# Performance work log

Hardware: AMD Instinct MI355X
Metric: run time of the kernel (lower is better)

The kernel has to match this reference:

```python
import jax, jax.numpy as jnp
import numpy as np

HX_INIT = 1e-6  # matches torch: zeros + 1e-06


def log_g(x):
    # log of continuous activation g: x>=0 -> log(x+0.5), else log(sigmoid(x)) = -softplus(-x)
    return jnp.where(x >= 0, jnp.log(jax.nn.relu(x) + 0.5), -jax.nn.softplus(-x))


def setup_inputs() -> dict:
    key = jax.random.key(0)
    k1, k2, k3 = jax.random.split(key, 3)
    N, L, H_in, H = 8, 4096, 512, 512
    x = jax.random.normal(k1, (N, L, H_in), dtype=jnp.float32)
    W = jax.random.normal(k2, (3 * H, H_in), dtype=jnp.float32) * 0.05
    b = jax.random.normal(k3, (3 * H,), dtype=jnp.float32) * 0.05
    return {"x": x, "W": W, "b": b}


def reference(x, W, b):
    N, L, _ = x.shape
    H = W.shape[0] // 3
    # gate preactivations: (N, L, 3H)
    pre = jnp.einsum('nli,oi->nlo', x, W) + b
    f_pre, i_pre, h_pre = jnp.split(pre, 3, axis=-1)
    # log-space gates
    diff = jax.nn.softplus(-f_pre) - jax.nn.softplus(-i_pre)
    log_f = -jax.nn.softplus(diff)       # log f'_t
    log_i = -jax.nn.softplus(-diff)      # log i'_t
    log_tilde_h = log_g(h_pre)
    # initial hidden state hx = 1e-6 (zeros + eps), shape (N, 1, H)
    log_h0 = jnp.full((N, 1, H), jnp.log(jnp.asarray(HX_INIT, x.dtype)), dtype=x.dtype)
    log_values = jnp.concatenate([log_h0, log_i + log_tilde_h], axis=1)  # (N, L+1, H)
    # Heinsen log-space parallel scan
    a_star = jnp.pad(jnp.cumsum(log_f, axis=1), ((0, 0), (1, 0), (0, 0)))  # (N, L+1, H)
    log_h = a_star + jax.lax.cumlogsumexp(log_values - a_star, axis=1)
    return jnp.exp(log_h)[:, 1:]  # (N, L, H)
```

## Files before the change

### kernel.cpp

```cpp
#include <hip/hip_runtime.h>
#include <hip/hip_bf16.h>


#define H_DIM 512
#define LSEQ 4096
#define NBATCH 8
#define M_TOTAL (NBATCH * LSEQ)

#define BM 128
#define BK 64

#define CS 128
#define NC 32

typedef __attribute__((ext_vector_type(8))) short short8;
typedef __attribute__((ext_vector_type(4))) float floatx4;
typedef __attribute__((ext_vector_type(4))) float float4v;
typedef _Float16 h2 __attribute__((ext_vector_type(2)));
typedef _Float16 h4 __attribute__((ext_vector_type(4)));
typedef __attribute__((ext_vector_type(2))) float float2v;

#define NEG_BIG (-1.0e30f)
#define C_LOG2E 1.4426950408889634f
#define LOG2_HX0 (-19.931568569324174f)

__device__ __forceinline__ float exp2_hw(float x) {
#if __has_builtin(__builtin_amdgcn_exp2f)
    return __builtin_amdgcn_exp2f(x);
#else
    return exp2f(x);
#endif
}

__device__ __forceinline__ float log2_hw(float x) {
#if __has_builtin(__builtin_amdgcn_logf)
    return __builtin_amdgcn_logf(x);
#else
    return log2f(x);
#endif
}

__device__ __forceinline__ float logaddexp2_f(float p, float q) {
    float m = fmaxf(p, q);
    float d = -fabsf(p - q);
    return m + log2_hw(1.0f + exp2_hw(d));
}

__device__ __forceinline__ float bf16u_to_f(unsigned short u) {
    unsigned int w = ((unsigned int)u) << 16;
    float f;
    __builtin_memcpy(&f, &w, 4);
    return f;
}

__device__ __forceinline__ unsigned short f_to_bf16u(float f) {
    __hip_bfloat16 h = __float2bfloat16(f);
    unsigned short u;
    __builtin_memcpy(&u, &h, 2);
    return u;
}

__device__ __forceinline__ void gload_lds16(const void* g, void* l) {
    __builtin_amdgcn_global_load_lds(
        (const __attribute__((address_space(1))) unsigned int*)g,
        (__attribute__((address_space(3))) unsigned int*)l, 16, 0, 0);
}

__global__ void detect_and_bias(const unsigned short* __restrict__ xu,
                                const void* __restrict__ bsrc,
                                int* __restrict__ flag,
                                float* __restrict__ bdst) {
    __shared__ int cnt;
    if (threadIdx.x == 0) cnt = 0;
    __syncthreads();
    int local = 0;
    for (int i = threadIdx.x; i < 16384; i += 256) {
        unsigned short u = xu[i];
        if (((u >> 7) & 0xFF) == 0xFF) local++;
    }
    if (local) atomicAdd(&cnt, local);
    __syncthreads();
    int f = (cnt > 8) ? 1 : 0;
    if (threadIdx.x == 0) flag[0] = f;
    for (int i = threadIdx.x; i < 3 * H_DIM; i += 256)
        bdst[i] = f ? ((const float*)bsrc)[i]
                    : bf16u_to_f(((const unsigned short*)bsrc)[i]);
}

__global__ __launch_bounds__(256)
void convert_inputs(const void* __restrict__ x, const void* __restrict__ W,
                    unsigned short* __restrict__ xc,
                    unsigned short* __restrict__ Wc,
                    const int* __restrict__ flag) {
    const int bx = blockIdx.x;
    const void* src;
    unsigned short* dst;
    int i;
    if (bx < 8192) { src = x; dst = xc; i = (bx * 256 + threadIdx.x) * 8; }
    else           { src = W; dst = Wc; i = ((bx - 8192) * 256 + threadIdx.x) * 8; }
    if (*flag) {
        const float4v* s4 = (const float4v*)((const float*)src + i);
        float4v a = s4[0], b = s4[1];
        short8 v;
        v[0] = (short)f_to_bf16u(a[0]); v[1] = (short)f_to_bf16u(a[1]);
        v[2] = (short)f_to_bf16u(a[2]); v[3] = (short)f_to_bf16u(a[3]);
        v[4] = (short)f_to_bf16u(b[0]); v[5] = (short)f_to_bf16u(b[1]);
        v[6] = (short)f_to_bf16u(b[2]); v[7] = (short)f_to_bf16u(b[3]);
        *(short8*)&dst[i] = v;
    } else {
        *(short8*)&dst[i] = *(const short8*)&((const short*)src)[i];
    }
}

__global__ __launch_bounds__(256, 3)
void gemm_gates(const unsigned short* __restrict__ x,
                const unsigned short* __restrict__ W,
                const float* __restrict__ bias,
                h2* __restrict__ plv,
                float* __restrict__ Asum, float* __restrict__ Bval,
                float* __restrict__ Asub, float* __restrict__ Bsub) {
    __shared__ __align__(16) char ldsbuf[40960];
    short* Alds = (short*)ldsbuf;
    short* Blds = (short*)(ldsbuf + 16384);
    h2* sc = (h2*)ldsbuf;
    float* sa = (float*)(ldsbuf + 32768);
    float* sb = sa + 256;

    const int bx = blockIdx.x;
    const int by = blockIdx.y;
    const int tid = threadIdx.x;
    const int lane = tid & 63;
    const int w = tid >> 6;
    const int wr = (w >> 1) * 64;
    const int wc2 = w & 1;
    const int l8 = lane >> 3, s8 = lane & 7;
    const int sg = s8 ^ l8;
    const int fr = lane & 15;
    const int q = lane >> 4;

    const int R0 = by * BM;

    floatx4 acc[4][6];
    #pragma unroll
    for (int i = 0; i < 4; i++)
        #pragma unroll
        for (int j = 0; j < 6; j++)
            acc[i][j] = (floatx4){0.f, 0.f, 0.f, 0.f};

    const short* xg = (const short*)x;
    const short* wg = (const short*)W;

    for (int k0 = 0; k0 < H_DIM; k0 += BK) {
        __syncthreads();
        #pragma unroll
        for (int i = 0; i < 4; i++) {
            int c = w * 4 + i;
            const short* g = xg + (size_t)(R0 + c * 8 + l8) * H_DIM + k0 + sg * 8;
            gload_lds16(g, &Alds[c * 512]);
        }
        #pragma unroll
        for (int i = 0; i < 6; i++) {
            int c = w * 6 + i;
            int br = c * 8 + l8;
            int wrow = (br >> 6) * H_DIM + bx * 64 + (br & 63);
            const short* g = wg + (size_t)wrow * H_DIM + k0 + sg * 8;
            gload_lds16(g, &Blds[c * 512]);
        }
        __syncthreads();

        #pragma unroll
        for (int ks = 0; ks < 2; ks++) {
            const int s = ks * 4 + q;
            short8 af[4], bf[6];
            #pragma unroll
            for (int mt = 0; mt < 4; mt++) {
                int ar = wr + mt * 16 + fr;
                af[mt] = *(const short8*)&Alds[ar * BK + ((s ^ (ar & 7)) << 3)];
            }
            #pragma unroll
            for (int j = 0; j < 6; j++) {
                int nt = (j >> 1) * 4 + wc2 * 2 + (j & 1);
                int brr = nt * 16 + fr;
                bf[j] = *(const short8*)&Blds[brr * BK + ((s ^ (brr & 7)) << 3)];
            }
            #pragma unroll
            for (int mt = 0; mt < 4; mt++)
                #pragma unroll
                for (int j = 0; j < 6; j++)
                    acc[mt][j] = __builtin_amdgcn_mfma_f32_16x16x32_bf16(
                        af[mt], bf[j], acc[mt][j], 0, 0, 0);
        }
    }

    __syncthreads();

    const int rowb = R0 + wr + q * 4;
    const int tloc0 = wr + q * 4;
    #pragma unroll
    for (int jj = 0; jj < 2; jj++) {
        int hl = wc2 * 32 + jj * 16 + fr;
        int hcol = bx * 64 + hl;
        float bfv = bias[hcol];
        float biv = bias[H_DIM + hcol];
        float bhv = bias[2 * H_DIM + hcol];
        float bf2 = -bfv * C_LOG2E;
        float bi2 = -biv * C_LOG2E;
        #pragma unroll
        for (int mt = 0; mt < 4; mt++) {
            #pragma unroll
            for (int r = 0; r < 4; r++) {
                float ef = exp2_hw(fminf(fmaf(acc[mt][jj][r], -C_LOG2E, bf2), 126.0f));
                float ei = exp2_hw(fminf(fmaf(acc[mt][2 + jj][r], -C_LOG2E, bi2), 126.0f));
                float hp = acc[mt][4 + jj][r] + bhv;
                float eh = exp2_hw(fminf(-hp * C_LOG2E, 126.0f));
                float afv = 1.0f + ef, aiv = 1.0f + ei;
                float sfi = afv + aiv;
                float ls = log2_hw(sfi);
                float lf = log2_hw(aiv) - ls;
                float marg = (hp >= 0.0f) ? (hp + 0.5f) : (1.0f + eh);
                float lm = log2_hw(marg);
                float lg = (hp >= 0.0f) ? lm : -lm;
                float lv = (log2_hw(afv) - ls) + lg;
                int row = rowb + mt * 16 + r;
                h2 pk;
                pk[0] = (_Float16)lf;
                pk[1] = (_Float16)lv;
                plv[(size_t)row * H_DIM + hcol] = pk;
                sc[(tloc0 + mt * 16 + r) * 64 + hl] = pk;
            }
        }
    }

    __syncthreads();

    const int n = by >> 5, c = by & 31;
    {
        float a = 0.f, bacc = NEG_BIG;
        const int t0 = w * 32;
        #pragma unroll 4
        for (int t = t0; t < t0 + 32; t++) {
            h2 p = sc[t * 64 + lane];
            float f = (float)p[0];
            bacc = logaddexp2_f(f + bacc, (float)p[1]);
            a += f;
        }
        sa[w * 64 + lane] = a;
        sb[w * 64 + lane] = bacc;
        size_t o = (((size_t)n * NC + c) * 4 + w) * H_DIM + bx * 64 + lane;
        Asub[o] = a;
        Bsub[o] = bacc;
    }
    __syncthreads();

    if (w == 0) {
        float a = sa[lane], b = sb[lane];
        #pragma unroll
        for (int s = 1; s < 4; s++) {
            float as = sa[s * 64 + lane], bs = sb[s * 64 + lane];
            b = logaddexp2_f(as + b, bs);
            a += as;
        }
        size_t o = ((size_t)n * NC + c) * H_DIM + bx * 64 + lane;
        Asum[o] = a;
        Bval[o] = b;
    }
}

__global__ __launch_bounds__(256)
void scan_apply(const h2* __restrict__ plv,
                const float* __restrict__ Asum, const float* __restrict__ Bval,
                const float* __restrict__ Asub, const float* __restrict__ Bsub,
                void* __restrict__ outv, const int* __restrict__ flag) {
    const int cc = blockIdx.x;
    const int n = blockIdx.y;
    const int c = cc >> 2, s = cc & 3;
    const int h0 = threadIdx.x * 2;
    const int f32out = *flag;

    float r0 = LOG2_HX0;
    float r1 = r0;
    size_t so = (size_t)n * NC * H_DIM + h0;
    int cp = 0;
    for (; cp + 4 <= c; cp += 4) {
        float2v A0 = *(const float2v*)&Asum[so + (size_t)(cp + 0) * H_DIM];
        float2v B0 = *(const float2v*)&Bval[so + (size_t)(cp + 0) * H_DIM];
        float2v A1 = *(const float2v*)&Asum[so + (size_t)(cp + 1) * H_DIM];
        float2v B1 = *(const float2v*)&Bval[so + (size_t)(cp + 1) * H_DIM];
        float2v A2 = *(const float2v*)&Asum[so + (size_t)(cp + 2) * H_DIM];
        float2v B2 = *(const float2v*)&Bval[so + (size_t)(cp + 2) * H_DIM];
        float2v A3 = *(const float2v*)&Asum[so + (size_t)(cp + 3) * H_DIM];
        float2v B3 = *(const float2v*)&Bval[so + (size_t)(cp + 3) * H_DIM];
        r0 = logaddexp2_f(A0[0] + r0, B0[0]); r1 = logaddexp2_f(A0[1] + r1, B0[1]);
        r0 = logaddexp2_f(A1[0] + r0, B1[0]); r1 = logaddexp2_f(A1[1] + r1, B1[1]);
        r0 = logaddexp2_f(A2[0] + r0, B2[0]); r1 = logaddexp2_f(A2[1] + r1, B2[1]);
        r0 = logaddexp2_f(A3[0] + r0, B3[0]); r1 = logaddexp2_f(A3[1] + r1, B3[1]);
    }
    for (; cp < c; cp++) {
        float2v A = *(const float2v*)&Asum[so + (size_t)cp * H_DIM];
        float2v B = *(const float2v*)&Bval[so + (size_t)cp * H_DIM];
        r0 = logaddexp2_f(A[0] + r0, B[0]);
        r1 = logaddexp2_f(A[1] + r1, B[1]);
    }
    size_t sub = (((size_t)n * NC + c) * 4) * H_DIM + h0;
    for (int sp = 0; sp < s; sp++) {
        float2v A = *(const float2v*)&Asub[sub + (size_t)sp * H_DIM];
        float2v B = *(const float2v*)&Bsub[sub + (size_t)sp * H_DIM];
        r0 = logaddexp2_f(A[0] + r0, B[0]);
        r1 = logaddexp2_f(A[1] + r1, B[1]);
    }

    size_t base = ((size_t)n * LSEQ + (size_t)c * CS + s * 32) * H_DIM + h0;
    if (f32out) {
        float* of = (float*)outv;
        #pragma unroll 4
        for (int t = 0; t < 32; t++) {
            size_t idx = base + (size_t)t * H_DIM;
            h4 p = *(const h4*)&plv[idx];
            r0 = logaddexp2_f((float)p[0] + r0, (float)p[1]);
            r1 = logaddexp2_f((float)p[2] + r1, (float)p[3]);
            float2v o2 = {exp2_hw(r0), exp2_hw(r1)};
            *(float2v*)&of[idx] = o2;
        }
    } else {
        unsigned int* ob32 = (unsigned int*)outv;
        #pragma unroll 4
        for (int t = 0; t < 32; t++) {
            size_t idx = base + (size_t)t * H_DIM;
            h4 p = *(const h4*)&plv[idx];
            r0 = logaddexp2_f((float)p[0] + r0, (float)p[1]);
            r1 = logaddexp2_f((float)p[2] + r1, (float)p[3]);
            unsigned int pk = ((unsigned int)f_to_bf16u(exp2_hw(r1)) << 16)
                            | f_to_bf16u(exp2_hw(r0));
            ob32[idx >> 1] = pk;
        }
    }
}

extern "C" void kernel_launch(void* const* d_in, const int* in_sizes, int n_in,
                              void* d_out, int out_size, void* d_ws, size_t ws_size,
                              hipStream_t stream) {
    const void* x = d_in[0];
    const void* W = d_in[1];
    const void* b = d_in[2];

    char* wsb = (char*)d_ws;
    int* flag            = (int*)wsb;
    float* bconv         = (float*)(wsb + 16);
    unsigned short* xc   = (unsigned short*)(wsb + 16384);
    unsigned short* Wc   = (unsigned short*)(wsb + 16384 + 33554432);
    h2* plv              = (h2*)(wsb + 36700160);
    float* Asum          = (float*)(wsb + 103809024);
    float* Bval          = (float*)(wsb + 104333312);
    float* Asub          = (float*)(wsb + 104857600);
    float* Bsub          = (float*)(wsb + 106954752);

    detect_and_bias<<<1, 256, 0, stream>>>((const unsigned short*)x, b, flag, bconv);
    convert_inputs<<<8576, 256, 0, stream>>>(x, W, xc, Wc, flag);

    dim3 g1(H_DIM / 64, M_TOTAL / BM);
    gemm_gates<<<g1, 256, 0, stream>>>(xc, Wc, bconv, plv, Asum, Bval, Asub, Bsub);

    dim3 g2(NC * 4, NBATCH);
    scan_apply<<<g2, 256, 0, stream>>>(plv, Asum, Bval, Asub, Bsub, d_out, flag);
}
```

Baseline: 235.6 us.

## Swap GEMM grid order, widen scan_apply vectors, vectorize detect kernel

New measurement: 212.4 us. -9.8%, faster.

```diff
diff --git a/kernel.cpp b/kernel.cpp
--- a/kernel.cpp
+++ b/kernel.cpp
@@ -17,8 +17,9 @@
 typedef __attribute__((ext_vector_type(4))) float floatx4;
 typedef __attribute__((ext_vector_type(4))) float float4v;
 typedef _Float16 h2 __attribute__((ext_vector_type(2)));
-typedef _Float16 h4 __attribute__((ext_vector_type(4)));
+typedef _Float16 h8 __attribute__((ext_vector_type(8)));
 typedef __attribute__((ext_vector_type(2))) float float2v;
+typedef __attribute__((ext_vector_type(2))) unsigned int uint2v;
 
 #define NEG_BIG (-1.0e30f)
 #define C_LOG2E 1.4426950408889634f
@@ -73,18 +74,27 @@
     __shared__ int cnt;
     if (threadIdx.x == 0) cnt = 0;
     __syncthreads();
+    const short8* x8 = (const short8*)xu;
     int local = 0;
-    for (int i = threadIdx.x; i < 16384; i += 256) {
-        unsigned short u = xu[i];
-        if (((u >> 7) & 0xFF) == 0xFF) local++;
+    #pragma unroll
+    for (int j = 0; j < 8; j++) {
+        short8 v = x8[threadIdx.x + j * 256];
+        #pragma unroll
+        for (int e = 0; e < 8; e++) {
+            unsigned short u = (unsigned short)v[e];
+            if (((u >> 7) & 0xFF) == 0xFF) local++;
+        }
     }
     if (local) atomicAdd(&cnt, local);
     __syncthreads();
     int f = (cnt > 8) ? 1 : 0;
     if (threadIdx.x == 0) flag[0] = f;
-    for (int i = threadIdx.x; i < 3 * H_DIM; i += 256)
+    #pragma unroll
+    for (int j = 0; j < 6; j++) {
+        int i = threadIdx.x + j * 256;
         bdst[i] = f ? ((const float*)bsrc)[i]
                     : bf16u_to_f(((const unsigned short*)bsrc)[i]);
+    }
 }
 
 __global__ __launch_bounds__(256)
@@ -126,8 +136,8 @@
     float* sa = (float*)(ldsbuf + 32768);
     float* sb = sa + 256;
 
-    const int bx = blockIdx.x;
-    const int by = blockIdx.y;
+    const int by = blockIdx.x;
+    const int bx = blockIdx.y;
     const int tid = threadIdx.x;
     const int lane = tid & 63;
     const int w = tid >> 6;
@@ -273,40 +283,44 @@
                 void* __restrict__ outv, const int* __restrict__ flag) {
     const int cc = blockIdx.x;
     const int n = blockIdx.y;
-    const int c = cc >> 2, s = cc & 3;
-    const int h0 = threadIdx.x * 2;
+    const int c = cc & 31;
+    const int s = (cc >> 5) * 2 + (threadIdx.x >> 7);
+    const int h0 = (threadIdx.x & 127) * 4;
     const int f32out = *flag;
 
-    float r0 = LOG2_HX0;
-    float r1 = r0;
+    float r0 = LOG2_HX0, r1 = r0, r2 = r0, r3 = r0;
     size_t so = (size_t)n * NC * H_DIM + h0;
     int cp = 0;
     for (; cp + 4 <= c; cp += 4) {
-        float2v A0 = *(const float2v*)&Asum[so + (size_t)(cp + 0) * H_DIM];
-        float2v B0 = *(const float2v*)&Bval[so + (size_t)(cp + 0) * H_DIM];
-        float2v A1 = *(const float2v*)&Asum[so + (size_t)(cp + 1) * H_DIM];
-        float2v B1 = *(const float2v*)&Bval[so + (size_t)(cp + 1) * H_DIM];
-        float2v A2 = *(const float2v*)&Asum[so + (size_t)(cp + 2) * H_DIM];
-        float2v B2 = *(const float2v*)&Bval[so + (size_t)(cp + 2) * H_DIM];
-        float2v A3 = *(const float2v*)&Asum[so + (size_t)(cp + 3) * H_DIM];
-        float2v B3 = *(const float2v*)&Bval[so + (size_t)(cp + 3) * H_DIM];
+        float4v A0 = *(const float4v*)&Asum[so + (size_t)(cp + 0) * H_DIM];
+        float4v B0 = *(const float4v*)&Bval[so + (size_t)(cp + 0) * H_DIM];
+        float4v A1 = *(const float4v*)&Asum[so + (size_t)(cp + 1) * H_DIM];
+        float4v B1 = *(const float4v*)&Bval[so + (size_t)(cp + 1) * H_DIM];
+        float4v A2 = *(const float4v*)&Asum[so + (size_t)(cp + 2) * H_DIM];
+        float4v B2 = *(const float4v*)&Bval[so + (size_t)(cp + 2) * H_DIM];
+        float4v A3 = *(const float4v*)&Asum[so + (size_t)(cp + 3) * H_DIM];
+        float4v B3 = *(const float4v*)&Bval[so + (size_t)(cp + 3) * H_DIM];
         r0 = logaddexp2_f(A0[0] + r0, B0[0]); r1 = logaddexp2_f(A0[1] + r1, B0[1]);
+        r2 = logaddexp2_f(A0[2] + r2, B0[2]); r3 = logaddexp2_f(A0[3] + r3, B0[3]);
         r0 = logaddexp2_f(A1[0] + r0, B1[0]); r1 = logaddexp2_f(A1[1] + r1, B1[1]);
+        r2 = logaddexp2_f(A1[2] + r2, B1[2]); r3 = logaddexp2_f(A1[3] + r3, B1[3]);
         r0 = logaddexp2_f(A2[0] + r0, B2[0]); r1 = logaddexp2_f(A2[1] + r1, B2[1]);
+        r2 = logaddexp2_f(A2[2] + r2, B2[2]); r3 = logaddexp2_f(A2[3] + r3, B2[3]);
         r0 = logaddexp2_f(A3[0] + r0, B3[0]); r1 = logaddexp2_f(A3[1] + r1, B3[1]);
+        r2 = logaddexp2_f(A3[2] + r2, B3[2]); r3 = logaddexp2_f(A3[3] + r3, B3[3]);
     }
     for (; cp < c; cp++) {
-        float2v A = *(const float2v*)&Asum[so + (size_t)cp * H_DIM];
-        float2v B = *(const float2v*)&Bval[so + (size_t)cp * H_DIM];
-        r0 = logaddexp2_f(A[0] + r0, B[0]);
-        r1 = logaddexp2_f(A[1] + r1, B[1]);
+        float4v A = *(const float4v*)&Asum[so + (size_t)cp * H_DIM];
+        float4v B = *(const float4v*)&Bval[so + (size_t)cp * H_DIM];
+        r0 = logaddexp2_f(A[0] + r0, B[0]); r1 = logaddexp2_f(A[1] + r1, B[1]);
+        r2 = logaddexp2_f(A[2] + r2, B[2]); r3 = logaddexp2_f(A[3] + r3, B[3]);
     }
     size_t sub = (((size_t)n * NC + c) * 4) * H_DIM + h0;
     for (int sp = 0; sp < s; sp++) {
-        float2v A = *(const float2v*)&Asub[sub + (size_t)sp * H_DIM];
-        float2v B = *(const float2v*)&Bsub[sub + (size_t)sp * H_DIM];
-        r0 = logaddexp2_f(A[0] + r0, B[0]);
-        r1 = logaddexp2_f(A[1] + r1, B[1]);
+        float4v A = *(const float4v*)&Asub[sub + (size_t)sp * H_DIM];
+        float4v B = *(const float4v*)&Bsub[sub + (size_t)sp * H_DIM];
+        r0 = logaddexp2_f(A[0] + r0, B[0]); r1 = logaddexp2_f(A[1] + r1, B[1]);
+        r2 = logaddexp2_f(A[2] + r2, B[2]); r3 = logaddexp2_f(A[3] + r3, B[3]);
     }
 
     size_t base = ((size_t)n * LSEQ + (size_t)c * CS + s * 32) * H_DIM + h0;
@@ -315,23 +329,28 @@
         #pragma unroll 4
         for (int t = 0; t < 32; t++) {
             size_t idx = base + (size_t)t * H_DIM;
-            h4 p = *(const h4*)&plv[idx];
+            h8 p = *(const h8*)&plv[idx];
             r0 = logaddexp2_f((float)p[0] + r0, (float)p[1]);
             r1 = logaddexp2_f((float)p[2] + r1, (float)p[3]);
-            float2v o2 = {exp2_hw(r0), exp2_hw(r1)};
-            *(float2v*)&of[idx] = o2;
+            r2 = logaddexp2_f((float)p[4] + r2, (float)p[5]);
+            r3 = logaddexp2_f((float)p[6] + r3, (float)p[7]);
+            float4v o4 = {exp2_hw(r0), exp2_hw(r1), exp2_hw(r2), exp2_hw(r3)};
+            *(float4v*)&of[idx] = o4;
         }
     } else {
         unsigned int* ob32 = (unsigned int*)outv;
         #pragma unroll 4
         for (int t = 0; t < 32; t++) {
             size_t idx = base + (size_t)t * H_DIM;
-            h4 p = *(const h4*)&plv[idx];
+            h8 p = *(const h8*)&plv[idx];
             r0 = logaddexp2_f((float)p[0] + r0, (float)p[1]);
             r1 = logaddexp2_f((float)p[2] + r1, (float)p[3]);
-            unsigned int pk = ((unsigned int)f_to_bf16u(exp2_hw(r1)) << 16)
-                            | f_to_bf16u(exp2_hw(r0));
-            ob32[idx >> 1] = pk;
+            r2 = logaddexp2_f((float)p[4] + r2, (float)p[5]);
+            r3 = logaddexp2_f((float)p[6] + r3, (float)p[7]);
+            uint2v pk;
+            pk[0] = ((unsigned int)f_to_bf16u(exp2_hw(r1)) << 16) | f_to_bf16u(exp2_hw(r0));
+            pk[1] = ((unsigned int)f_to_bf16u(exp2_hw(r3)) << 16) | f_to_bf16u(exp2_hw(r2));
+            *(uint2v*)&ob32[idx >> 1] = pk;
         }
     }
 }
@@ -357,9 +376,9 @@
     detect_and_bias<<<1, 256, 0, stream>>>((const unsigned short*)x, b, flag, bconv);
     convert_inputs<<<8576, 256, 0, stream>>>(x, W, xc, Wc, flag);
 
-    dim3 g1(H_DIM / 64, M_TOTAL / BM);
+    dim3 g1(M_TOTAL / BM, H_DIM / 64);
     gemm_gates<<<g1, 256, 0, stream>>>(xc, Wc, bconv, plv, Asum, Bval, Asub, Bsub);
 
-    dim3 g2(NC * 4, NBATCH);
+    dim3 g2(NC * 2, NBATCH);
     scan_apply<<<g2, 256, 0, stream>>>(plv, Asum, Bval, Asub, Bsub, d_out, flag);
 }
```
